# Kernel tuning notes

Hardware: AMD Instinct MI355X
Metric: run time of the kernel (lower is better)

## Reference

```python
import jax, jax.numpy as jnp
import numpy as np


def setup_inputs() -> dict:
    T, B, D = 2048, 8, 1024
    key = jax.random.key(0)
    k1, k2, k3 = jax.random.split(key, 3)
    # xavier-uniform-ish scale for [D, D] weights
    lim = float(np.sqrt(6.0 / (D + D)))
    return {
        "x": jax.random.normal(k1, (T, B, D), dtype=jnp.float32),
        "h0": jnp.zeros((B, D), dtype=jnp.float32),
        "W_alpha": jax.random.uniform(k2, (D, D), dtype=jnp.float32, minval=-lim, maxval=lim),
        "b_alpha": jnp.full((D,), 2.0, dtype=jnp.float32),  # init_alpha_bias
        "W_x": jax.random.uniform(k3, (D, D), dtype=jnp.float32, minval=-lim, maxval=lim),
        "b": jnp.zeros((D,), dtype=jnp.float32),
    }


def reference(x, h0, W_alpha, b_alpha, W_x, b):
    # Precompute input projections for all timesteps (one big GEMM each).
    # alpha_t = sigmoid(W_alpha @ x_t + b_alpha); v_t = tanh(h_{t-1} + W_x @ x_t + b)
    alpha_all = jax.nn.sigmoid(jnp.einsum('tbd,ed->tbe', x, W_alpha) + b_alpha)  # [T,B,D]
    wx_all = jnp.einsum('tbd,ed->tbe', x, W_x) + b                                # [T,B,D]

    def step(h_prev, inp):
        alpha, wx = inp
        v = jnp.tanh(h_prev + wx)
        h_new = alpha * h_prev + (1.0 - alpha) * v
        out = h_new * jax.nn.silu(h_new)
        return h_new, (out, h_new)

    _, (output, hs) = jax.lax.scan(step, h0, (alpha_all, wx_all))
    h = jnp.concatenate([h0[None], hs], axis=0)  # [T+1, B, D]
    return output, h
```

## Files before the change

### kernel.cpp

```cpp
#include <hip/hip_runtime.h>
#include <hip/hip_bf16.h>
#include <cstdint>
#include <cstddef>

#define T_STEPS 2048
#define BATCH   8
#define D_DIM   1024
#define M_ROWS  (T_STEPS * BATCH)
#define N_COLS  (2 * D_DIM)
#define K_DIM   D_DIM
#define NCH     (BATCH * D_DIM)

#define BM 128
#define BN 128
#define BK 32

typedef __bf16 bf16x8 __attribute__((ext_vector_type(8)));
typedef float  f32x4  __attribute__((ext_vector_type(4)));

__device__ __forceinline__ unsigned short f2bf_rne(float f) {
    union { float f; unsigned u; } c; c.f = f;
    unsigned u = c.u;
    u += 0x7fffu + ((u >> 16) & 1u);
    return (unsigned short)(u >> 16);
}

__device__ __forceinline__ float sigmoid_f(float z) {
    return 1.0f / (1.0f + __expf(-z));
}

__device__ __forceinline__ void glds16(const void* gptr, void* lptr) {
    __builtin_amdgcn_global_load_lds(
        (const __attribute__((address_space(1))) unsigned int*)gptr,
        (__attribute__((address_space(3))) unsigned int*)lptr,
        16, 0, 0);
}

__global__ void cvt_bf16_kernel(const float* __restrict__ src,
                                unsigned short* __restrict__ dst, int n4) {
    int i = blockIdx.x * blockDim.x + threadIdx.x;
    if (i >= n4) return;
    float4 v = reinterpret_cast<const float4*>(src)[i];
    ushort4 o;
    o.x = f2bf_rne(v.x); o.y = f2bf_rne(v.y);
    o.z = f2bf_rne(v.z); o.w = f2bf_rne(v.w);
    reinterpret_cast<ushort4*>(dst)[i] = o;
}

__global__ __launch_bounds__(256, 2)
void gemm_kernel(const unsigned short* __restrict__ A,
                 const unsigned short* __restrict__ Bm,
                 const float* __restrict__ b_alpha,
                 const float* __restrict__ b_x,
                 float* __restrict__ alpha_out,
                 float* __restrict__ wx_out)
{
    __shared__ unsigned short sA[BM * BK];
    __shared__ unsigned short sB[BN * BK];

    const int tid  = threadIdx.x;
    const int wave = tid >> 6;
    const int lane = tid & 63;

    const int orig = blockIdx.y * 16 + blockIdx.x;
    const int swz  = (orig & 7) * 256 + (orig >> 3);
    const int rowBase = (swz >> 4) * BM;
    const int colBase = (swz & 15) * BN;

    const int wr = (wave >> 1) * 64;
    const int wc = (wave & 1) * 64;

    const int laneHi = lane >> 4;
    const int laneLo = lane & 15;

    const int dRow = lane >> 2;
    const int dCol = (lane & 3) * 8;

    f32x4 acc[4][4];
#pragma unroll
    for (int i = 0; i < 4; i++)
#pragma unroll
        for (int j = 0; j < 4; j++)
            acc[i][j] = (f32x4)(0.0f);

    for (int k0 = 0; k0 < K_DIM; k0 += BK) {
#pragma unroll
        for (int p = 0; p < 2; ++p) {
            const int seg = wave * 2 + p;
            glds16(A + (size_t)(rowBase + seg * 16 + dRow) * K_DIM + k0 + dCol,
                   &sA[seg * 512]);
            glds16(Bm + (size_t)(colBase + seg * 16 + dRow) * K_DIM + k0 + dCol,
                   &sB[seg * 512]);
        }
        __syncthreads();

        bf16x8 af[4], bfr[4];
#pragma unroll
        for (int i = 0; i < 4; i++)
            af[i] = *reinterpret_cast<const bf16x8*>(
                &sA[(wr + i * 16 + laneLo) * BK + laneHi * 8]);
#pragma unroll
        for (int j = 0; j < 4; j++)
            bfr[j] = *reinterpret_cast<const bf16x8*>(
                &sB[(wc + j * 16 + laneLo) * BK + laneHi * 8]);
        __syncthreads();

#pragma unroll
        for (int i = 0; i < 4; i++)
#pragma unroll
            for (int j = 0; j < 4; j++)
                acc[i][j] = __builtin_amdgcn_mfma_f32_16x16x32_bf16(
                    af[i], bfr[j], acc[i][j], 0, 0, 0);
    }

#pragma unroll
    for (int i = 0; i < 4; i++) {
        int row = rowBase + wr + i * 16 + laneHi * 4;
#pragma unroll
        for (int j = 0; j < 4; j++) {
            int col = colBase + wc + j * 16 + laneLo;
            if (col < D_DIM) {
                float bias = b_alpha[col];
#pragma unroll
                for (int r = 0; r < 4; r++) {
                    float z = acc[i][j][r] + bias;
                    alpha_out[(size_t)(row + r) * D_DIM + col] = sigmoid_f(z);
                }
            } else {
                int c2 = col - D_DIM;
                float bias = b_x[c2];
#pragma unroll
                for (int r = 0; r < 4; r++)
                    wx_out[(size_t)(row + r) * D_DIM + c2] = acc[i][j][r] + bias;
            }
        }
    }
}

#define TT  32
#define NT  (T_STEPS / TT)
#define PF  3

__global__ __launch_bounds__(192)
void scan_kernel(const float* __restrict__ alpha,
                 const float* __restrict__ wx,
                 const float* __restrict__ h0,
                 float* __restrict__ out,
                 float* __restrict__ hout)
{
    __shared__ float sIn[4][2][TT * 64];
    __shared__ float sH[2][TT * 64];

    const int lane = threadIdx.x & 63;
    const int wid  = threadIdx.x >> 6;
    const int ch0  = blockIdx.x * 64;

    const float C2L = 2.88539008177792681472f;

    const int q  = lane >> 4;
    const int c4 = (lane & 15) * 4;

    const int tq  = lane >> 4;
    const int c4s = (lane & 15) * 4;

    float h = 0.0f;

    if (wid == 1) {
#pragma unroll
        for (int t = 0; t < PF; ++t)
#pragma unroll
            for (int p = 0; p < TT / 4; ++p) {
                const size_t g = (size_t)(t * TT + p * 4 + q) * NCH + ch0 + c4;
                glds16(alpha + g, &sIn[t][0][p * 256]);
                glds16(wx    + g, &sIn[t][1][p * 256]);
            }
        asm volatile("s_waitcnt vmcnt(32)" ::: "memory");
    } else if (wid == 0) {
        h = h0[ch0 + lane];
    } else {
        hout[ch0 + lane] = h0[ch0 + lane];
    }
    __builtin_amdgcn_s_barrier();
    __builtin_amdgcn_sched_barrier(0);

    for (int tile = 0; tile < NT; ++tile) {
        if (wid == 0) {
            const float* sA  = &sIn[tile & 3][0][0];
            const float* sW  = &sIn[tile & 3][1][0];
            float* sHc       = &sH[tile & 1][0];
#pragma unroll 8
            for (int ts = 0; ts < TT; ++ts) {
                const float a = sA[ts * 64 + lane];
                const float w = sW[ts * 64 + lane];
                const float u = 1.0f - a;
                const float p = (h + w) * C2L;
                const float e = __builtin_amdgcn_exp2f(p);
                const float r = __builtin_amdgcn_rcpf(e + 1.0f);
                const float m = fmaf(a, h, u);
                h = fmaf(-(u + u), r, m);
                sHc[ts * 64 + lane] = h;
            }
            asm volatile("s_waitcnt lgkmcnt(0)" ::: "memory");
            __builtin_amdgcn_sched_barrier(0);
        } else if (wid == 1) {
            if (tile + PF < NT) {
                const int b  = (tile + PF) & 3;
                const int t0 = (tile + PF) * TT;
#pragma unroll
                for (int p = 0; p < TT / 4; ++p) {
                    const size_t g = (size_t)(t0 + p * 4 + q) * NCH + ch0 + c4;
                    glds16(alpha + g, &sIn[b][0][p * 256]);
                    glds16(wx    + g, &sIn[b][1][p * 256]);
                }
            }
            if (tile + PF < NT) {
                asm volatile("s_waitcnt vmcnt(32)" ::: "memory");
            } else if (tile + PF == NT) {
                asm volatile("s_waitcnt vmcnt(16)" ::: "memory");
            } else if (tile + 1 < NT) {
                asm volatile("s_waitcnt vmcnt(0)" ::: "memory");
            }
            __builtin_amdgcn_sched_barrier(0);
        } else {
            if (tile >= 1) {
                const float* sHs = &sH[(tile - 1) & 1][0];
                const int tb = (tile - 1) * TT;
#pragma unroll
                for (int i = 0; i < TT / 4; ++i) {
                    const int tsrow = i * 4 + tq;
                    const float4 hv = *reinterpret_cast<const float4*>(
                        &sHs[tsrow * 64 + c4s]);
                    *reinterpret_cast<float4*>(
                        &hout[(size_t)(tb + tsrow + 1) * NCH + ch0 + c4s]) = hv;
                    float4 o;
                    o.x = hv.x * hv.x * sigmoid_f(hv.x);
                    o.y = hv.y * hv.y * sigmoid_f(hv.y);
                    o.z = hv.z * hv.z * sigmoid_f(hv.z);
                    o.w = hv.w * hv.w * sigmoid_f(hv.w);
                    *reinterpret_cast<float4*>(
                        &out[(size_t)(tb + tsrow) * NCH + ch0 + c4s]) = o;
                }
            }
        }
        __builtin_amdgcn_s_barrier();
        __builtin_amdgcn_sched_barrier(0);
    }

    if (wid == 2) {
        const float* sHs = &sH[(NT - 1) & 1][0];
        const int tb = (NT - 1) * TT;
#pragma unroll
        for (int i = 0; i < TT / 4; ++i) {
            const int tsrow = i * 4 + tq;
            const float4 hv = *reinterpret_cast<const float4*>(
                &sHs[tsrow * 64 + c4s]);
            *reinterpret_cast<float4*>(
                &hout[(size_t)(tb + tsrow + 1) * NCH + ch0 + c4s]) = hv;
            float4 o;
            o.x = hv.x * hv.x * sigmoid_f(hv.x);
            o.y = hv.y * hv.y * sigmoid_f(hv.y);
            o.z = hv.z * hv.z * sigmoid_f(hv.z);
            o.w = hv.w * hv.w * sigmoid_f(hv.w);
            *reinterpret_cast<float4*>(
                &out[(size_t)(tb + tsrow) * NCH + ch0 + c4s]) = o;
        }
    }
}

extern "C" void kernel_launch(void* const* d_in, const int* in_sizes, int n_in,
                              void* d_out, int out_size, void* d_ws, size_t ws_size,
                              hipStream_t stream) {
    const float* x       = (const float*)d_in[0];
    const float* h0      = (const float*)d_in[1];
    const float* W_alpha = (const float*)d_in[2];
    const float* b_alpha = (const float*)d_in[3];
    const float* W_x     = (const float*)d_in[4];
    const float* b       = (const float*)d_in[5];

    float* out  = (float*)d_out;
    float* hout = out + (size_t)T_STEPS * BATCH * D_DIM;

    float* ws_alpha = (float*)d_ws;
    float* ws_wx    = ws_alpha + (size_t)M_ROWS * D_DIM;
    unsigned short* ws_x = (unsigned short*)(ws_wx + (size_t)M_ROWS * D_DIM);
    unsigned short* ws_W = ws_x + (size_t)M_ROWS * K_DIM;

    {
        int n4 = M_ROWS * K_DIM / 4;
        cvt_bf16_kernel<<<(n4 + 255) / 256, 256, 0, stream>>>(x, ws_x, n4);
    }
    {
        int n4 = D_DIM * K_DIM / 4;
        cvt_bf16_kernel<<<(n4 + 255) / 256, 256, 0, stream>>>(W_alpha, ws_W, n4);
        cvt_bf16_kernel<<<(n4 + 255) / 256, 256, 0, stream>>>(
            W_x, ws_W + (size_t)D_DIM * K_DIM, n4);
    }

    {
        dim3 grid(N_COLS / BN, M_ROWS / BM);
        gemm_kernel<<<grid, 256, 0, stream>>>(ws_x, ws_W, b_alpha, b,
                                              ws_alpha, ws_wx);
    }

    scan_kernel<<<NCH / 64, 192, 0, stream>>>(ws_alpha, ws_wx, h0, out, hout);
}
```

Before: 362.1 us.

## Halve channels per scan block, deepen prefetch ring, pad shared h buffer

```diff
diff --git a/kernel.cpp b/kernel.cpp
--- a/kernel.cpp
+++ b/kernel.cpp
@@ -137,9 +137,11 @@
     }
 }
 
-#define TT  32
-#define NT  (T_STEPS / TT)
-#define PF  3
+#define TT   32
+#define NT   (T_STEPS / TT)
+#define PF   6
+#define CPB  32
+#define SHS  36
 
 __global__ __launch_bounds__(192)
 void scan_kernel(const float* __restrict__ alpha,
@@ -148,20 +150,17 @@
                  float* __restrict__ out,
                  float* __restrict__ hout)
 {
-    __shared__ float sIn[4][2][TT * 64];
-    __shared__ float sH[2][TT * 64];
+    __shared__ float sIn[8][2][TT * CPB];
+    __shared__ float sH[2][TT * SHS];
 
     const int lane = threadIdx.x & 63;
     const int wid  = threadIdx.x >> 6;
-    const int ch0  = blockIdx.x * 64;
+    const int ch0  = blockIdx.x * CPB;
 
     const float C2L = 2.88539008177792681472f;
 
-    const int q  = lane >> 4;
-    const int c4 = (lane & 15) * 4;
-
-    const int tq  = lane >> 4;
-    const int c4s = (lane & 15) * 4;
+    const int q8 = lane >> 3;
+    const int c4 = (lane & 7) * 4;
 
     float h = 0.0f;
 
@@ -169,56 +168,67 @@
 #pragma unroll
         for (int t = 0; t < PF; ++t)
 #pragma unroll
-            for (int p = 0; p < TT / 4; ++p) {
-                const size_t g = (size_t)(t * TT + p * 4 + q) * NCH + ch0 + c4;
+            for (int p = 0; p < TT / 8; ++p) {
+                const size_t g = (size_t)(t * TT + p * 8 + q8) * NCH + ch0 + c4;
                 glds16(alpha + g, &sIn[t][0][p * 256]);
                 glds16(wx    + g, &sIn[t][1][p * 256]);
             }
-        asm volatile("s_waitcnt vmcnt(32)" ::: "memory");
+        asm volatile("s_waitcnt vmcnt(40)" ::: "memory");
     } else if (wid == 0) {
-        h = h0[ch0 + lane];
+        if (lane < CPB) h = h0[ch0 + lane];
     } else {
-        hout[ch0 + lane] = h0[ch0 + lane];
+        if (lane < CPB) hout[ch0 + lane] = h0[ch0 + lane];
     }
     __builtin_amdgcn_s_barrier();
     __builtin_amdgcn_sched_barrier(0);
 
     for (int tile = 0; tile < NT; ++tile) {
         if (wid == 0) {
-            const float* sA  = &sIn[tile & 3][0][0];
-            const float* sW  = &sIn[tile & 3][1][0];
+            const float* sA  = &sIn[tile & 7][0][0];
+            const float* sW  = &sIn[tile & 7][1][0];
             float* sHc       = &sH[tile & 1][0];
+            if (lane < CPB) {
 #pragma unroll 8
-            for (int ts = 0; ts < TT; ++ts) {
-                const float a = sA[ts * 64 + lane];
-                const float w = sW[ts * 64 + lane];
-                const float u = 1.0f - a;
-                const float p = (h + w) * C2L;
-                const float e = __builtin_amdgcn_exp2f(p);
-                const float r = __builtin_amdgcn_rcpf(e + 1.0f);
-                const float m = fmaf(a, h, u);
-                h = fmaf(-(u + u), r, m);
-                sHc[ts * 64 + lane] = h;
+                for (int ts = 0; ts < TT; ++ts) {
+                    const float a = sA[ts * CPB + lane];
+                    const float w = sW[ts * CPB + lane];
+                    const float u = 1.0f - a;
+                    const float p = (h + w) * C2L;
+                    const float e = __builtin_amdgcn_exp2f(p);
+                    const float r = __builtin_amdgcn_rcpf(e + 1.0f);
+                    const float m = fmaf(a, h, u);
+                    h = fmaf(-(u + u), r, m);
+                    sHc[ts * SHS + lane] = h;
+                }
             }
             asm volatile("s_waitcnt lgkmcnt(0)" ::: "memory");
             __builtin_amdgcn_sched_barrier(0);
         } else if (wid == 1) {
             if (tile + PF < NT) {
-                const int b  = (tile + PF) & 3;
+                const int b  = (tile + PF) & 7;
                 const int t0 = (tile + PF) * TT;
 #pragma unroll
-                for (int p = 0; p < TT / 4; ++p) {
-                    const size_t g = (size_t)(t0 + p * 4 + q) * NCH + ch0 + c4;
+                for (int p = 0; p < TT / 8; ++p) {
+                    const size_t g = (size_t)(t0 + p * 8 + q8) * NCH + ch0 + c4;
                     glds16(alpha + g, &sIn[b][0][p * 256]);
                     glds16(wx    + g, &sIn[b][1][p * 256]);
                 }
             }
-            if (tile + PF < NT) {
-                asm volatile("s_waitcnt vmcnt(32)" ::: "memory");
-            } else if (tile + PF == NT) {
-                asm volatile("s_waitcnt vmcnt(16)" ::: "memory");
-            } else if (tile + 1 < NT) {
-                asm volatile("s_waitcnt vmcnt(0)" ::: "memory");
+            {
+                const int rem = NT - 1 - tile;
+                if (rem >= PF) {
+                    asm volatile("s_waitcnt vmcnt(40)" ::: "memory");
+                } else if (rem == 5) {
+                    asm volatile("s_waitcnt vmcnt(32)" ::: "memory");
+                } else if (rem == 4) {
+                    asm volatile("s_waitcnt vmcnt(24)" ::: "memory");
+                } else if (rem == 3) {
+                    asm volatile("s_waitcnt vmcnt(16)" ::: "memory");
+                } else if (rem == 2) {
+                    asm volatile("s_waitcnt vmcnt(8)" ::: "memory");
+                } else if (rem == 1) {
+                    asm volatile("s_waitcnt vmcnt(0)" ::: "memory");
+                }
             }
             __builtin_amdgcn_sched_barrier(0);
         } else {
@@ -226,19 +236,19 @@
                 const float* sHs = &sH[(tile - 1) & 1][0];
                 const int tb = (tile - 1) * TT;
 #pragma unroll
-                for (int i = 0; i < TT / 4; ++i) {
-                    const int tsrow = i * 4 + tq;
+                for (int i = 0; i < TT / 8; ++i) {
+                    const int tsrow = i * 8 + q8;
                     const float4 hv = *reinterpret_cast<const float4*>(
-                        &sHs[tsrow * 64 + c4s]);
+                        &sHs[tsrow * SHS + c4]);
                     *reinterpret_cast<float4*>(
-                        &hout[(size_t)(tb + tsrow + 1) * NCH + ch0 + c4s]) = hv;
+                        &hout[(size_t)(tb + tsrow + 1) * NCH + ch0 + c4]) = hv;
                     float4 o;
                     o.x = hv.x * hv.x * sigmoid_f(hv.x);
                     o.y = hv.y * hv.y * sigmoid_f(hv.y);
                     o.z = hv.z * hv.z * sigmoid_f(hv.z);
                     o.w = hv.w * hv.w * sigmoid_f(hv.w);
                     *reinterpret_cast<float4*>(
-                        &out[(size_t)(tb + tsrow) * NCH + ch0 + c4s]) = o;
+                        &out[(size_t)(tb + tsrow) * NCH + ch0 + c4]) = o;
                 }
             }
         }
@@ -250,19 +260,19 @@
         const float* sHs = &sH[(NT - 1) & 1][0];
         const int tb = (NT - 1) * TT;
 #pragma unroll
-        for (int i = 0; i < TT / 4; ++i) {
-            const int tsrow = i * 4 + tq;
+        for (int i = 0; i < TT / 8; ++i) {
+            const int tsrow = i * 8 + q8;
             const float4 hv = *reinterpret_cast<const float4*>(
-                &sHs[tsrow * 64 + c4s]);
+                &sHs[tsrow * SHS + c4]);
             *reinterpret_cast<float4*>(
-                &hout[(size_t)(tb + tsrow + 1) * NCH + ch0 + c4s]) = hv;
+                &hout[(size_t)(tb + tsrow + 1) * NCH + ch0 + c4]) = hv;
             float4 o;
             o.x = hv.x * hv.x * sigmoid_f(hv.x);
             o.y = hv.y * hv.y * sigmoid_f(hv.y);
             o.z = hv.z * hv.z * sigmoid_f(hv.z);
             o.w = hv.w * hv.w * sigmoid_f(hv.w);
             *reinterpret_cast<float4*>(
-                &out[(size_t)(tb + tsrow) * NCH + ch0 + c4s]) = o;
+                &out[(size_t)(tb + tsrow) * NCH + ch0 + c4]) = o;
         }
     }
 }
@@ -302,5 +312,5 @@
                                               ws_alpha, ws_wx);
     }
 
-    scan_kernel<<<NCH / 64, 192, 0, stream>>>(ws_alpha, ws_wx, h0, out, hout);
-}
+    scan_kernel<<<NCH / CPB, 192, 0, stream>>>(ws_alpha, ws_wx, h0, out, hout);
+}
```

After: 360.8 us. No clear change (-0.4%).
